# Optimization experiments

Hardware: AMD Instinct MI355X
Metric: run time of the kernel (lower is better)

The kernel has to match this reference:

```python
import jax, jax.numpy as jnp
import numpy as np

EPS_LN = 1e-12
EPS_BN = 1e-5


def layernorm(x, w, b):
    u = jnp.mean(x, axis=-1, keepdims=True)
    s = jnp.mean((x - u) ** 2, axis=-1, keepdims=True)
    return w * ((x - u) / jnp.sqrt(s + EPS_LN)) + b


def reps_block(x, ln1_w, ln1_b, lin_w, lin_b, ln2_w, ln2_b):
    # GRAPHLayerNorm -> (dropout, identity in eval) -> Linear -> ReLU -> GRAPHLayerNorm
    h = layernorm(x, ln1_w, ln1_b)
    h = jax.nn.relu(jnp.einsum('bnd,od->bno', h, lin_w) + lin_b)
    return layernorm(h, ln2_w, ln2_b)


def attend(x):
    # full dense self-attention: softmax(x x^T) x ; dropout is identity in eval
    scores = jnp.einsum('bnd,bmd->bnm', x, x)  # [B,4096,4096]
    attn = jax.nn.softmax(scores, axis=-1)
    return jnp.einsum('bnm,bmd->bnd', attn, x)


def setup_inputs() -> dict:
    key = jax.random.key(0)
    ks = jax.random.split(key, 8)
    B, C, H, W = 4, 512, 64, 64
    D = 512
    inp = {
        'T1': jax.random.normal(ks[0], (B, C, H, W), jnp.float32),
        'T2': jax.random.normal(ks[1], (B, C, H, W), jnp.float32),
        'w_conv3': jax.random.normal(ks[2], (1024, 1024, 3, 3), jnp.float32) * 0.01,
        'w_conv1': jax.random.normal(ks[3], (512, 1024, 1, 1), jnp.float32) * 0.03,
        'bn_gamma': jnp.ones((512,), jnp.float32),
        'bn_beta': jnp.zeros((512,), jnp.float32),
        'bn_mean': jnp.zeros((512,), jnp.float32),
        'bn_var': jnp.ones((512,), jnp.float32),
        'ln1_w': jnp.ones((D,), jnp.float32),
        'ln1_b': jnp.zeros((D,), jnp.float32),
        'lin_w': jax.random.normal(ks[4], (D, D), jnp.float32) * 0.04,
        'lin_b': jnp.zeros((D,), jnp.float32),
        'ln2_w': jnp.ones((D,), jnp.float32),
        'ln2_b': jnp.zeros((D,), jnp.float32),
    }
    return inp


def reference(T1, T2, w_conv3, w_conv1, bn_gamma, bn_beta, bn_mean, bn_var,
              ln1_w, ln1_b, lin_w, lin_b, ln2_w, ln2_b):
    B = T1.shape[0]
    X = jnp.concatenate((T1, T2), axis=1)  # [B,1024,64,64]
    dn = ('NCHW', 'OIHW', 'NCHW')
    X = jax.lax.conv_general_dilated(X, w_conv3, (1, 1), ((1, 1), (1, 1)), dimension_numbers=dn)
    X = jax.lax.conv_general_dilated(X, w_conv1, (1, 1), ((0, 0), (0, 0)), dimension_numbers=dn)  # [B,512,64,64]
    # BatchNorm (eval, running stats) + ReLU
    inv = (bn_gamma / jnp.sqrt(bn_var + EPS_BN))[None, :, None, None]
    X = jax.nn.relu(X * inv + (bn_beta - bn_mean * bn_gamma / jnp.sqrt(bn_var + EPS_BN))[None, :, None, None])
    x = X.transpose(0, 2, 3, 1).reshape(B, 4096, 512)
    # block 1
    rel = attend(x)
    rel = reps_block(x + rel, ln1_w, ln1_b, lin_w, lin_b, ln2_w, ln2_b)
    # block 2 (original code reuses self.reps_graph, i.e. SAME params)
    rel1 = attend(rel)
    rel1 = reps_block(rel + rel1, ln1_w, ln1_b, lin_w, lin_b, ln2_w, ln2_b)
    return rel1.reshape(B, 64, 64, 512).transpose(0, 3, 1, 2)  # [B,512,64,64]
```

## Files before the change

### kernel.cpp

```cpp
#include <hip/hip_runtime.h>
#include <stdint.h>

typedef float f32x4 __attribute__((ext_vector_type(4)));
typedef __bf16 bf16x8 __attribute__((ext_vector_type(8)));
typedef unsigned short u16;
typedef unsigned short u16x8 __attribute__((ext_vector_type(8)));

__device__ __forceinline__ float bf2f(u16 u){ unsigned int i = ((unsigned int)u)<<16; float f; __builtin_memcpy(&f,&i,4); return f; }
__device__ __forceinline__ u16 f2bf(float f){ unsigned int i; __builtin_memcpy(&i,&f,4); i += 0x7FFFu + ((i>>16)&1u); return (u16)(i>>16); }
__device__ __forceinline__ u16 f2h(float f){ _Float16 h = (_Float16)f; u16 b; __builtin_memcpy(&b,&h,2); return b; }
__device__ __forceinline__ float h2f(u16 b){ _Float16 h; __builtin_memcpy(&h,&b,2); return (float)h; }

__device__ __forceinline__ void gld16(const void* g, void* l){
  __builtin_amdgcn_global_load_lds(
      (const __attribute__((address_space(1))) void*)(uintptr_t)g,
      (__attribute__((address_space(3))) void*)(unsigned int)(uintptr_t)l, 16, 0, 0);
}

__global__ __launch_bounds__(256) void pad_interior(const float* __restrict__ T1,
                                                    const float* __restrict__ T2,
                                                    u16* __restrict__ Xpad){
  const int n = blockIdx.z, ct = blockIdx.y, pt = blockIdx.x;
  const int t = threadIdx.x;
  const int c0 = ct*64, p0 = pt*64;
  const float* src = (c0 < 512) ? (T1 + ((long)n*512 + c0)*4096)
                                : (T2 + ((long)n*512 + (c0-512))*4096);
  __shared__ u16 lds[64][66];
  #pragma unroll
  for (int i=0;i<4;i++){
    int c = i*16 + (t>>4);
    int ch = t&15;
    float4 v = *(const float4*)(src + (long)c*4096 + p0 + ch*4);
    int p = ch*4;
    lds[p+0][c] = f2bf(v.x); lds[p+1][c] = f2bf(v.y);
    lds[p+2][c] = f2bf(v.z); lds[p+3][c] = f2bf(v.w);
  }
  __syncthreads();
  #pragma unroll
  for (int i=0;i<8;i++){
    int p = i*8 + (t>>5);
    int c2 = t&31;
    int pix = p0 + p; int yy = (pix>>6)+1, xx = (pix&63)+1;
    ushort2 val; val.x = lds[p][2*c2]; val.y = lds[p][2*c2+1];
    *(ushort2*)(Xpad + (((long)n*66 + yy)*66 + xx)*1024 + c0 + 2*c2) = val;
  }
}

__global__ __launch_bounds__(256) void prep_w3(const float* __restrict__ w3, u16* __restrict__ wk3t){
  const int o = blockIdx.x; const int t = threadIdx.x;
  __shared__ u16 lds[9216];
  const float* src = w3 + (long)o*9216;
  #pragma unroll
  for (int i=0;i<9;i++){
    int j = i*256 + t;
    float4 v = *(const float4*)(src + j*4);
    lds[j*4+0]=f2bf(v.x); lds[j*4+1]=f2bf(v.y); lds[j*4+2]=f2bf(v.z); lds[j*4+3]=f2bf(v.w);
  }
  __syncthreads();
  u16* dst = wk3t + (long)o*9216;
  #pragma unroll
  for (int i=0;i<36;i++){
    int j = i*256 + t; int tp = j>>10, ci = j&1023;
    dst[j] = lds[ci*9+tp];
  }
}

__global__ void prep_w1(const float* __restrict__ w1, const float* __restrict__ bg,
                        const float* __restrict__ bv, u16* __restrict__ w1t){
  long i = (long)blockIdx.x*256 + threadIdx.x;
  int o = (int)(i>>10);
  float inv = bg[o] / sqrtf(bv[o] + 1e-5f);
  w1t[i] = f2bf(w1[i]*inv);
}

__global__ void prep_bias1(const float* __restrict__ bg, const float* __restrict__ bb,
                           const float* __restrict__ bm, const float* __restrict__ bv,
                           float* __restrict__ bias1){
  int o = blockIdx.x*256+threadIdx.x;
  float inv = bg[o]/sqrtf(bv[o]+1e-5f);
  bias1[o] = bb[o] - bm[o]*inv;
}

__global__ void cvt_bf(const float* __restrict__ s, u16* __restrict__ d){
  long i = (long)blockIdx.x*256 + threadIdx.x;
  d[i] = f2bf(s[i]);
}

__global__ __launch_bounds__(256) void row_norm(const u16* __restrict__ x, float* __restrict__ nrm){
  const int row = blockIdx.x*4 + (threadIdx.x>>6);
  const int lane = threadIdx.x & 63;
  u16x8 q = *(const u16x8*)(x + (long)row*512 + lane*8);
  float s = 0.f;
  #pragma unroll
  for (int j=0;j<8;j++){ float f = bf2f(q[j]); s += f*f; }
  #pragma unroll
  for (int off=32; off; off>>=1) s += __shfl_xor(s, off);
  if (lane==0) nrm[row] = s;
}

__global__ __launch_bounds__(256) void transpose_bf(const u16* __restrict__ src, u16* __restrict__ dst,
                                                    int R, int C, long sStr, long dStr){
  const int z = blockIdx.z;
  src += (long)z*sStr; dst += (long)z*dStr;
  const int r0 = blockIdx.x*64, c0 = blockIdx.y*64;
  const int t = threadIdx.x;
  __shared__ u16 lds[64][66];
  #pragma unroll
  for (int i=0;i<4;i++){
    int r = i*16 + (t>>4), ch = t&15;
    ushort4 v = *(const ushort4*)(src + (long)(r0+r)*C + c0 + ch*4);
    lds[r][ch*4+0]=v.x; lds[r][ch*4+1]=v.y; lds[r][ch*4+2]=v.z; lds[r][ch*4+3]=v.w;
  }
  __syncthreads();
  #pragma unroll
  for (int i=0;i<4;i++){
    int c = i*16 + (t>>4), ch = t&15;
    ushort4 v;
    v.x = lds[ch*4+0][c]; v.y = lds[ch*4+1][c]; v.z = lds[ch*4+2][c]; v.w = lds[ch*4+3][c];
    *(ushort4*)(dst + (long)(c0+c)*R + r0 + ch*4) = v;
  }
}

__global__ __launch_bounds__(256) void transpose_bf_f32(const u16* __restrict__ src, float* __restrict__ dst){
  const int z = blockIdx.z;
  src += (long)z*4096*512; dst += (long)z*512*4096;
  const int r0 = blockIdx.x*64, c0 = blockIdx.y*64;
  const int t = threadIdx.x;
  __shared__ u16 lds[64][66];
  #pragma unroll
  for (int i=0;i<4;i++){
    int r = i*16 + (t>>4), ch = t&15;
    ushort4 v = *(const ushort4*)(src + (long)(r0+r)*512 + c0 + ch*4);
    lds[r][ch*4+0]=v.x; lds[r][ch*4+1]=v.y; lds[r][ch*4+2]=v.z; lds[r][ch*4+3]=v.w;
  }
  __syncthreads();
  #pragma unroll
  for (int i=0;i<4;i++){
    int c = i*16 + (t>>4), ch = t&15;
    float4 v;
    v.x = bf2f(lds[ch*4+0][c]); v.y = bf2f(lds[ch*4+1][c]);
    v.z = bf2f(lds[ch*4+2][c]); v.w = bf2f(lds[ch*4+3][c]);
    *(float4*)(dst + (long)(c0+c)*4096 + r0 + ch*4) = v;
  }
}

template<int EPI, int CONV>
__global__ __launch_bounds__(512, 2) void gemm256(
    const u16* __restrict__ A, const u16* __restrict__ Bt, void* __restrict__ Cv,
    int K, int lda, int ldb, int ldc, const float* __restrict__ srow)
{
  extern __shared__ u16 sm[];
  const int t = threadIdx.x;
  const int lane = t & 63;
  const int wid = t >> 6;
  const int wr = wid >> 2, wc = wid & 3;

  const int orig = blockIdx.y * gridDim.x + blockIdx.x;
  const int cpx = (gridDim.x * gridDim.y) >> 3;
  const int swz = (orig & 7) * cpx + (orig >> 3);
  const int bx = swz % gridDim.x;
  const int by = swz / gridDim.x;
  const long m0 = (long)by * 256, n0 = (long)bx * 256;

  const int row0 = t >> 2;
  const int cs0  = (t & 3) ^ ((row0 >> 1) & 3);

  const u16 *aB0, *aB1;
  if (CONV) {
    long m_ = m0 + row0;
    long pb0 = ((long)((int)(m_>>12)*66 + (int)((m_>>6)&63)))*66 + (int)(m_&63);
    m_ = m0 + row0 + 128;
    long pb1 = ((long)((int)(m_>>12)*66 + (int)((m_>>6)&63)))*66 + (int)(m_&63);
    aB0 = A + pb0*1024 + cs0*8;
    aB1 = A + pb1*1024 + cs0*8;
  } else {
    aB0 = A + (m0 + row0)*(long)lda + cs0*8;
    aB1 = A + (m0 + row0 + 128)*(long)lda + cs0*8;
  }
  const u16* bB0 = Bt + (n0 + row0)*(long)ldb + cs0*8;
  const u16* bB1 = Bt + (n0 + row0 + 128)*(long)ldb + cs0*8;

  auto issueA = [&](int sub, long aoff){
    u16* d = sm + sub*8192 + t*8;
    gld16(aB0 + aoff, d);
    gld16(aB1 + aoff, d + 4096);
  };
  auto issueB = [&](int sub, long boff){
    u16* d = sm + 32768 + sub*8192 + t*8;
    gld16(bB0 + boff, d);
    gld16(bB1 + boff, d + 4096);
  };
  auto conv_aoff = [&](int tile)->long {
    int kb = tile << 6;
    int tap = kb >> 10;
    int cb  = kb & 1023;
    int ky = (tap >= 6) ? 2 : (tap >= 3 ? 1 : 0);
    int kx = tap - ky*3;
    return (long)(ky*66 + kx)*1024 + cb;
  };

  const int frow = lane & 15;
  const int elemoff = (((lane>>4) ^ ((frow>>1)&3)) << 3);
  const int rAoff = (wr*128 + frow)*32 + elemoff;
  const int rBoff = (wc*64  + frow)*32 + elemoff;

  f32x4 acc[8][4] = {};

  {
    long a0 = CONV ? conv_aoff(0) : 0L;
    issueA(0, a0);
    issueB(0, 0);
    issueA(1, a0 + 32);
    issueB(1, 32);
  }

  const int NT = K >> 6;
  for (int tile = 0; tile < NT; ++tile) {
    const int b = tile & 1;
    const int nb2 = b ^ 1;
    const bool lastT = (tile == NT-1);
    long aoffN = 0, boffN = 0;
    if (!lastT) {
      aoffN = CONV ? conv_aoff(tile+1) : (long)(tile+1)*64;
      boffN = (long)(tile+1)*64;
    }

    asm volatile("s_waitcnt vmcnt(4)" ::: "memory");
    __builtin_amdgcn_s_barrier();
    __builtin_amdgcn_sched_barrier(0);

    {
      const u16* pA = sm + (b*2+0)*8192 + rAoff;
      const u16* pB = sm + 32768 + (b*2+0)*8192 + rBoff;
      bf16x8 bf[4];
      #pragma unroll
      for (int i=0;i<4;i++) bf[i] = *(const bf16x8*)(pB + i*512);
      {
        bf16x8 a[4];
        #pragma unroll
        for (int i=0;i<4;i++) a[i] = *(const bf16x8*)(pA + i*512);
        if (!lastT) issueA(nb2*2+0, aoffN);
        __builtin_amdgcn_s_setprio(1);
        #pragma unroll
        for (int mi=0;mi<4;mi++)
          #pragma unroll
          for (int ni=0;ni<4;ni++)
            acc[mi][ni] = __builtin_amdgcn_mfma_f32_16x16x32_bf16(a[mi], bf[ni], acc[mi][ni],0,0,0);
        __builtin_amdgcn_s_setprio(0);
      }
      {
        bf16x8 a[4];
        #pragma unroll
        for (int i=0;i<4;i++) a[i] = *(const bf16x8*)(pA + (4+i)*512);
        if (!lastT) issueB(nb2*2+0, boffN);
        __builtin_amdgcn_s_setprio(1);
        #pragma unroll
        for (int mi=0;mi<4;mi++)
          #pragma unroll
          for (int ni=0;ni<4;ni++)
            acc[4+mi][ni] = __builtin_amdgcn_mfma_f32_16x16x32_bf16(a[mi], bf[ni], acc[4+mi][ni],0,0,0);
        __builtin_amdgcn_s_setprio(0);
      }
    }

    if (lastT) asm volatile("s_waitcnt vmcnt(0)" ::: "memory");
    else       asm volatile("s_waitcnt vmcnt(4)" ::: "memory");
    __builtin_amdgcn_s_barrier();
    __builtin_amdgcn_sched_barrier(0);

    {
      const u16* pA = sm + (b*2+1)*8192 + rAoff;
      const u16* pB = sm + 32768 + (b*2+1)*8192 + rBoff;
      bf16x8 bf[4];
      #pragma unroll
      for (int i=0;i<4;i++) bf[i] = *(const bf16x8*)(pB + i*512);
      {
        bf16x8 a[4];
        #pragma unroll
        for (int i=0;i<4;i++) a[i] = *(const bf16x8*)(pA + i*512);
        if (!lastT) issueA(nb2*2+1, aoffN + 32);
        __builtin_amdgcn_s_setprio(1);
        #pragma unroll
        for (int mi=0;mi<4;mi++)
          #pragma unroll
          for (int ni=0;ni<4;ni++)
            acc[mi][ni] = __builtin_amdgcn_mfma_f32_16x16x32_bf16(a[mi], bf[ni], acc[mi][ni],0,0,0);
        __builtin_amdgcn_s_setprio(0);
      }
      {
        bf16x8 a[4];
        #pragma unroll
        for (int i=0;i<4;i++) a[i] = *(const bf16x8*)(pA + (4+i)*512);
        if (!lastT) issueB(nb2*2+1, boffN + 32);
        __builtin_amdgcn_s_setprio(1);
        #pragma unroll
        for (int mi=0;mi<4;mi++)
          #pragma unroll
          for (int ni=0;ni<4;ni++)
            acc[4+mi][ni] = __builtin_amdgcn_mfma_f32_16x16x32_bf16(a[mi], bf[ni], acc[4+mi][ni],0,0,0);
        __builtin_amdgcn_s_setprio(0);
      }
    }
  }

  const int crow0 = wr*128 + ((lane>>4)<<2);
  const int ccol0 = wc*64 + frow;
  #pragma unroll
  for (int mi=0;mi<8;mi++){
    #pragma unroll
    for (int ni=0;ni<4;ni++){
      long col = n0 + ccol0 + ni*16;
      #pragma unroll
      for (int r=0;r<4;r++){
        long row = m0 + crow0 + mi*16 + r;
        float v = acc[mi][ni][r];
        if (EPI==3) ((u16*)Cv)[row*(long)ldc + col] = f2h(v - srow[row]);
        else        ((u16*)Cv)[row*(long)ldc + col] = f2bf(v);
      }
    }
  }
}

template<int EPI>
__global__ __launch_bounds__(256, 2) void gemm_bt(
    const u16* __restrict__ A, const u16* __restrict__ Bt,
    void* __restrict__ Cv, const float* __restrict__ bias,
    int K, int lda, int ldb, int ldc)
{
  const int t = threadIdx.x;
  const int lane = t & 63;
  const int w = t >> 6;
  const int wr = w >> 1, wc = w & 1;
  const long m0 = (long)blockIdx.y * 128;
  const long n0 = (long)blockIdx.x * 128;

  __shared__ u16 lA[128*32];
  __shared__ u16 lB[128*32];

  const u16* aS0 = A + (m0 + (t>>2))*(long)lda + (t&3)*8;
  const u16* aS1 = aS0 + 64*(long)lda;
  const u16* bS0 = Bt + (n0 + (t>>2))*(long)ldb + (t&3)*8;
  const u16* bS1 = bS0 + 64*(long)ldb;
  u16* dA0 = lA + t*8; u16* dA1 = lA + 2048 + t*8;
  u16* dB0 = lB + t*8; u16* dB1 = lB + 2048 + t*8;

  f32x4 acc[4][4] = {};
  const int frow = lane & 15, kq = (lane >> 4) * 8;
  const u16* rA = lA + (wr*64 + frow)*32 + kq;
  const u16* rB = lB + (wc*64 + frow)*32 + kq;

  for (int kb = 0; kb < K; kb += 32) {
    gld16(aS0 + kb, dA0); gld16(aS1 + kb, dA1);
    gld16(bS0 + kb, dB0); gld16(bS1 + kb, dB1);
    __syncthreads();
    bf16x8 af[4], bfr[4];
    #pragma unroll
    for (int i=0;i<4;i++) af[i]  = *(const bf16x8*)(rA + i*512);
    #pragma unroll
    for (int i=0;i<4;i++) bfr[i] = *(const bf16x8*)(rB + i*512);
    #pragma unroll
    for (int mi=0;mi<4;mi++)
      #pragma unroll
      for (int ni=0;ni<4;ni++)
        acc[mi][ni] = __builtin_amdgcn_mfma_f32_16x16x32_bf16(af[mi], bfr[ni], acc[mi][ni], 0,0,0);
    __syncthreads();
  }

  const int crow0 = wr*64 + ((lane>>4)<<2);
  const int ccol0 = wc*64 + (lane&15);
  #pragma unroll
  for (int mi=0;mi<4;mi++){
    #pragma unroll
    for (int ni=0;ni<4;ni++){
      long col = n0 + ccol0 + ni*16;
      float bv = (EPI==1) ? bias[col] : 0.0f;
      #pragma unroll
      for (int r=0;r<4;r++){
        long row = m0 + crow0 + mi*16 + r;
        float v = acc[mi][ni][r];
        if (EPI==1){ v += bv; v = v > 0.0f ? v : 0.0f; }
        ((u16*)Cv)[row*(long)ldc + col] = f2bf(v);
      }
    }
  }
}

__global__ __launch_bounds__(256, 2) void pv_gemm(
    const u16* __restrict__ P0, const u16* __restrict__ P1,
    const u16* __restrict__ P2, const u16* __restrict__ P3,
    const u16* __restrict__ xT, u16* __restrict__ attb)
{
  const int L = blockIdx.x;
  const int xcd = L & 7;
  const int z = xcd >> 1;
  const int tile = ((L >> 3) << 1) + (xcd & 1);
  const int bx = tile & 3, by = tile >> 2;
  const long ZS = 4096L*512;
  const u16* A  = (z==0)?P0:(z==1)?P1:(z==2)?P2:P3;
  const u16* Bt = xT   + (long)z*ZS;
  u16*       C  = attb + (long)z*ZS;
  const int K = 4096, lda = 4096, ldb = 4096, ldc = 512;

  const int t = threadIdx.x;
  const int lane = t & 63;
  const int w = t >> 6;
  const int wr = w >> 1, wc = w & 1;
  const long m0 = (long)by * 128;
  const long n0 = (long)bx * 128;

  __shared__ u16 lA[128*32];
  __shared__ u16 lB[128*32];

  const u16* aS0 = A + (m0 + (t>>2))*(long)lda + (t&3)*8;
  const u16* aS1 = aS0 + 64*(long)lda;
  const u16* bS0 = Bt + (n0 + (t>>2))*(long)ldb + (t&3)*8;
  const u16* bS1 = bS0 + 64*(long)ldb;
  u16* dA0 = lA + t*8; u16* dA1 = lA + 2048 + t*8;
  u16* dB0 = lB + t*8; u16* dB1 = lB + 2048 + t*8;

  f32x4 acc[4][4] = {};
  const int frow = lane & 15, kq = (lane >> 4) * 8;
  const u16* rA = lA + (wr*64 + frow)*32 + kq;
  const u16* rB = lB + (wc*64 + frow)*32 + kq;

  for (int kb = 0; kb < K; kb += 32) {
    gld16(aS0 + kb, dA0); gld16(aS1 + kb, dA1);
    gld16(bS0 + kb, dB0); gld16(bS1 + kb, dB1);
    __syncthreads();
    bf16x8 af[4], bfr[4];
    #pragma unroll
    for (int i=0;i<4;i++) af[i]  = *(const bf16x8*)(rA + i*512);
    #pragma unroll
    for (int i=0;i<4;i++) bfr[i] = *(const bf16x8*)(rB + i*512);
    #pragma unroll
    for (int mi=0;mi<4;mi++)
      #pragma unroll
      for (int ni=0;ni<4;ni++)
        acc[mi][ni] = __builtin_amdgcn_mfma_f32_16x16x32_bf16(af[mi], bfr[ni], acc[mi][ni], 0,0,0);
    __syncthreads();
  }

  const int crow0 = wr*64 + ((lane>>4)<<2);
  const int ccol0 = wc*64 + (lane&15);
  #pragma unroll
  for (int mi=0;mi<4;mi++){
    #pragma unroll
    for (int ni=0;ni<4;ni++){
      long col = n0 + ccol0 + ni*16;
      #pragma unroll
      for (int r=0;r<4;r++){
        long row = m0 + crow0 + mi*16 + r;
        C[row*(long)ldc + col] = f2bf(acc[mi][ni][r]);
      }
    }
  }
}

__global__ __launch_bounds__(256) void softmax_row(const u16* __restrict__ S, u16* __restrict__ P){
  const long row = blockIdx.x;
  const u16* src = S + row*4096;
  const int t = threadIdx.x, lane = t&63, w = t>>6;
  float v[16];
  #pragma unroll
  for (int i=0;i<2;i++){
    u16x8 q = *(const u16x8*)(src + t*16 + i*8);
    #pragma unroll
    for (int j=0;j<8;j++) v[i*8+j] = h2f(q[j]);
  }
  float mx = v[0];
  #pragma unroll
  for (int i=1;i<16;i++) mx = fmaxf(mx, v[i]);
  #pragma unroll
  for (int off=32; off; off>>=1) mx = fmaxf(mx, __shfl_xor(mx, off));
  __shared__ float red[4];
  if (lane==0) red[w] = mx;
  __syncthreads();
  mx = fmaxf(fmaxf(red[0],red[1]), fmaxf(red[2],red[3]));
  float sum = 0.0f;
  #pragma unroll
  for (int i=0;i<16;i++){ v[i] = __expf(v[i]-mx); sum += v[i]; }
  #pragma unroll
  for (int off=32; off; off>>=1) sum += __shfl_xor(sum, off);
  __shared__ float red2[4];
  if (lane==0) red2[w] = sum;
  __syncthreads();
  sum = red2[0]+red2[1]+red2[2]+red2[3];
  const float inv = 1.0f/sum;
  u16* dst = P + row*4096;
  #pragma unroll
  for (int i=0;i<2;i++){
    u16x8 o;
    #pragma unroll
    for (int j=0;j<8;j++) o[j] = f2bf(v[i*8+j]*inv);
    *(u16x8*)(dst + t*16 + i*8) = o;
  }
}

template<int ADD>
__global__ __launch_bounds__(256) void ln_row(
    const u16* __restrict__ X, const u16* __restrict__ Y,
    const float* __restrict__ w, const float* __restrict__ b,
    u16* __restrict__ outB)
{
  const long row = blockIdx.x;
  const int t = threadIdx.x, lane = t&63, wv = t>>6;
  ushort2 xv = *(const ushort2*)(X + row*512 + t*2);
  float v0 = bf2f(xv.x), v1 = bf2f(xv.y);
  if (ADD){
    ushort2 yv = *(const ushort2*)(Y + row*512 + t*2);
    v0 += bf2f(yv.x); v1 += bf2f(yv.y);
  }
  float s = v0+v1, q = v0*v0 + v1*v1;
  #pragma unroll
  for (int off=32; off; off>>=1){ s += __shfl_xor(s,off); q += __shfl_xor(q,off); }
  __shared__ float red[8];
  if (lane==0){ red[wv]=s; red[4+wv]=q; }
  __syncthreads();
  s = red[0]+red[1]+red[2]+red[3];
  q = red[4]+red[5]+red[6]+red[7];
  const float u = s*(1.0f/512.0f);
  const float var = q*(1.0f/512.0f) - u*u;
  const float inv = rsqrtf(var + 1e-12f);
  const int c = t*2;
  float o0 = (v0-u)*inv*w[c]   + b[c];
  float o1 = (v1-u)*inv*w[c+1] + b[c+1];
  ushort2 ov; ov.x=f2bf(o0); ov.y=f2bf(o1);
  *(ushort2*)(outB + row*512 + c) = ov;
}

extern "C" void kernel_launch(void* const* d_in, const int* in_sizes, int n_in,
                              void* d_out, int out_size, void* d_ws, size_t ws_size,
                              hipStream_t stream) {
  const float* T1   = (const float*)d_in[0];
  const float* T2   = (const float*)d_in[1];
  const float* w3   = (const float*)d_in[2];
  const float* w1   = (const float*)d_in[3];
  const float* bg   = (const float*)d_in[4];
  const float* bb   = (const float*)d_in[5];
  const float* bm   = (const float*)d_in[6];
  const float* bv   = (const float*)d_in[7];
  const float* ln1w = (const float*)d_in[8];
  const float* ln1b = (const float*)d_in[9];
  const float* linw = (const float*)d_in[10];
  const float* linb = (const float*)d_in[11];
  const float* ln2w = (const float*)d_in[12];
  const float* ln2b = (const float*)d_in[13];

  hipFuncSetAttribute(reinterpret_cast<const void*>(gemm256<0,1>),
                      hipFuncAttributeMaxDynamicSharedMemorySize, 131072);
  hipFuncSetAttribute(reinterpret_cast<const void*>(gemm256<3,0>),
                      hipFuncAttributeMaxDynamicSharedMemorySize, 131072);

  char* ws = (char*)d_ws;
  size_t off = 0;
  auto alloc = [&](size_t bytes)->char* {
    char* p = ws + off;
    off += (bytes + 255) & ~(size_t)255;
    return p;
  };
  const size_t XPAD_B = 4L*66*66*1024*2;
  u16*   Xpad  = (u16*)  alloc(XPAD_B);
  u16*   wk3t  = (u16*)  alloc(1024L*9216*2);
  u16*   w1t   = (u16*)  alloc(512L*1024*2);
  u16*   lint  = (u16*)  alloc(512L*512*2);
  float* bias1 = (float*)alloc(512*4);
  float* nrm   = (float*)alloc(16384L*4);
  u16*   Y1    = (u16*)  alloc(16384L*1024*2);
  u16*   x0    = (u16*)  alloc(16384L*512*2);
  u16*   xT    = (u16*)  alloc(4L*512*4096*2);
  u16*   Sreg  = (u16*)  alloc(2L*4096*4096*2);
  u16*   attb  = (u16*)  alloc(16384L*512*2);
  u16*   h     = (u16*)  alloc(16384L*512*2);
  u16*   g     = (u16*)  alloc(16384L*512*2);
  u16*   rel1  = (u16*)  alloc(16384L*512*2);
  u16*   Sh    = Sreg;
  u16*   P0    = Y1;
  u16*   P1    = h;
  u16*   P2    = Sreg + 4096L*4096;
  u16*   P3    = Xpad;
  if (off > ws_size) return;

  const long ZS = 4096L*512;

  hipMemsetAsync(Xpad, 0, XPAD_B, stream);
  pad_interior<<<dim3(64,16,4), 256, 0, stream>>>(T1, T2, Xpad);
  prep_w3<<<1024, 256, 0, stream>>>(w3, wk3t);
  prep_w1<<<2048, 256, 0, stream>>>(w1, bg, bv, w1t);
  prep_bias1<<<2, 256, 0, stream>>>(bg, bb, bm, bv, bias1);
  cvt_bf<<<1024, 256, 0, stream>>>(linw, lint);

  gemm256<0,1><<<dim3(4,64), 512, 131072, stream>>>(Xpad, wk3t, (void*)Y1, 9216, 0, 9216, 1024,
                                                    nullptr);
  gemm_bt<1><<<dim3(4,128), 256, 0, stream>>>(Y1, w1t, (void*)x0, bias1, 1024, 1024, 1024, 512);

  u16* Pz[4] = {P0, P1, P2, P3};
  auto attend = [&](const u16* xin){
    transpose_bf<<<dim3(64,8,4), 256, 0, stream>>>(xin, xT, 4096, 512, ZS, ZS);
    row_norm<<<4096, 256, 0, stream>>>(xin, nrm);
    for (int z=0; z<4; z++){
      const u16* xz = xin + (long)z*ZS;
      gemm256<3,0><<<dim3(16,16), 512, 131072, stream>>>(xz, xz, (void*)Sh, 512, 512, 512, 4096,
                                                         nrm + (long)z*4096);
      softmax_row<<<4096, 256, 0, stream>>>(Sh, Pz[z]);
    }
    pv_gemm<<<512, 256, 0, stream>>>(P0, P1, P2, P3, xT, attb);
  };

  attend(x0);
  ln_row<1><<<16384, 256, 0, stream>>>(x0, attb, ln1w, ln1b, h);
  gemm_bt<1><<<dim3(4,128), 256, 0, stream>>>(h, lint, (void*)g, linb, 512, 512, 512, 512);
  ln_row<0><<<16384, 256, 0, stream>>>(g, nullptr, ln2w, ln2b, rel1);

  attend(rel1);
  ln_row<1><<<16384, 256, 0, stream>>>(rel1, attb, ln1w, ln1b, h);
  gemm_bt<1><<<dim3(4,128), 256, 0, stream>>>(h, lint, (void*)g, linb, 512, 512, 512, 512);
  ln_row<0><<<16384, 256, 0, stream>>>(g, nullptr, ln2w, ln2b, x0);

  transpose_bf_f32<<<dim3(64,8,4), 256, 0, stream>>>(x0, (float*)d_out);
}
```

Measured before the change: 911.2 us.

## Pipeline PV GEMM with multi-buffered async LDS loads and swizzled layout

Rewrites the P·V GEMM main loop to prefetch the next K-tiles into a four-slot LDS ring (64 KB dynamic shared memory) using async global-to-LDS loads. It synchronises with vmcnt waits and raw barriers instead of two __syncthreads per step. An XOR swizzle on the LDS column chunks is meant to reduce bank conflicts, and s_setprio brackets the MFMA blocks. The goal is to hide global load latency behind MFMA work. The cost is more LDS per block, which may limit occupancy, plus hand-managed wait counts that must stay correct.

```diff
diff --git a/kernel.cpp b/kernel.cpp
--- a/kernel.cpp
+++ b/kernel.cpp
@@ -385,11 +385,12 @@
   }
 }
 
-__global__ __launch_bounds__(256, 2) void pv_gemm(
+__global__ __launch_bounds__(256, 2) void pv5(
     const u16* __restrict__ P0, const u16* __restrict__ P1,
     const u16* __restrict__ P2, const u16* __restrict__ P3,
     const u16* __restrict__ xT, u16* __restrict__ attb)
 {
+  extern __shared__ u16 pm[];
   const int L = blockIdx.x;
   const int xcd = L & 7;
   const int z = xcd >> 1;
@@ -399,49 +400,129 @@
   const u16* A  = (z==0)?P0:(z==1)?P1:(z==2)?P2:P3;
   const u16* Bt = xT   + (long)z*ZS;
   u16*       C  = attb + (long)z*ZS;
-  const int K = 4096, lda = 4096, ldb = 4096, ldc = 512;
+  const long m0 = (long)by * 128, n0 = (long)bx * 128;
 
   const int t = threadIdx.x;
   const int lane = t & 63;
   const int w = t >> 6;
   const int wr = w >> 1, wc = w & 1;
-  const long m0 = (long)by * 128;
-  const long n0 = (long)bx * 128;
-
-  __shared__ u16 lA[128*32];
-  __shared__ u16 lB[128*32];
-
-  const u16* aS0 = A + (m0 + (t>>2))*(long)lda + (t&3)*8;
-  const u16* aS1 = aS0 + 64*(long)lda;
-  const u16* bS0 = Bt + (n0 + (t>>2))*(long)ldb + (t&3)*8;
-  const u16* bS1 = bS0 + 64*(long)ldb;
-  u16* dA0 = lA + t*8; u16* dA1 = lA + 2048 + t*8;
-  u16* dB0 = lB + t*8; u16* dB1 = lB + 2048 + t*8;
+
+  const int row0 = t >> 2;
+  const int cs0  = (t & 3) ^ ((row0 >> 1) & 3);
+
+  const u16* aB0 = A + (m0 + row0)*4096L + cs0*8;
+  const u16* aB1 = aB0 + 64*4096L;
+  const u16* bB0 = Bt + (n0 + row0)*4096L + cs0*8;
+  const u16* bB1 = bB0 + 64*4096L;
+
+  auto issueA = [&](int sub, long off){
+    u16* d = pm + sub*4096 + t*8;
+    gld16(aB0 + off, d);
+    gld16(aB1 + off, d + 2048);
+  };
+  auto issueB = [&](int sub, long off){
+    u16* d = pm + 16384 + sub*4096 + t*8;
+    gld16(bB0 + off, d);
+    gld16(bB1 + off, d + 2048);
+  };
+
+  const int frow = lane & 15;
+  const int elemoff = (((lane>>4) ^ ((frow>>1)&3)) << 3);
+  const int rAoff = (wr*64 + frow)*32 + elemoff;
+  const int rBoff = (wc*64 + frow)*32 + elemoff;
 
   f32x4 acc[4][4] = {};
-  const int frow = lane & 15, kq = (lane >> 4) * 8;
-  const u16* rA = lA + (wr*64 + frow)*32 + kq;
-  const u16* rB = lB + (wc*64 + frow)*32 + kq;
-
-  for (int kb = 0; kb < K; kb += 32) {
-    gld16(aS0 + kb, dA0); gld16(aS1 + kb, dA1);
-    gld16(bS0 + kb, dB0); gld16(bS1 + kb, dB1);
-    __syncthreads();
-    bf16x8 af[4], bfr[4];
-    #pragma unroll
-    for (int i=0;i<4;i++) af[i]  = *(const bf16x8*)(rA + i*512);
-    #pragma unroll
-    for (int i=0;i<4;i++) bfr[i] = *(const bf16x8*)(rB + i*512);
-    #pragma unroll
-    for (int mi=0;mi<4;mi++)
+
+  issueA(0, 0);  issueB(0, 0);
+  issueA(1, 32); issueB(1, 32);
+
+  const int NT = 64;
+  for (int tl = 0; tl < NT; ++tl) {
+    const int b = tl & 1;
+    const int nb2 = b ^ 1;
+    const bool lastT = (tl == NT-1);
+    const long offN = (long)(tl+1)*64;
+
+    asm volatile("s_waitcnt vmcnt(4)" ::: "memory");
+    __builtin_amdgcn_s_barrier();
+    __builtin_amdgcn_sched_barrier(0);
+
+    {
+      const u16* pA = pm + (b*2+0)*4096 + rAoff;
+      const u16* pB = pm + 16384 + (b*2+0)*4096 + rBoff;
+      bf16x8 bf[4];
       #pragma unroll
-      for (int ni=0;ni<4;ni++)
-        acc[mi][ni] = __builtin_amdgcn_mfma_f32_16x16x32_bf16(af[mi], bfr[ni], acc[mi][ni], 0,0,0);
-    __syncthreads();
+      for (int i=0;i<4;i++) bf[i] = *(const bf16x8*)(pB + i*512);
+      {
+        bf16x8 a[2];
+        #pragma unroll
+        for (int i=0;i<2;i++) a[i] = *(const bf16x8*)(pA + i*512);
+        if (!lastT) issueA(nb2*2+0, offN);
+        __builtin_amdgcn_s_setprio(1);
+        #pragma unroll
+        for (int mi=0;mi<2;mi++)
+          #pragma unroll
+          for (int ni=0;ni<4;ni++)
+            acc[mi][ni] = __builtin_amdgcn_mfma_f32_16x16x32_bf16(a[mi], bf[ni], acc[mi][ni],0,0,0);
+        __builtin_amdgcn_s_setprio(0);
+      }
+      {
+        bf16x8 a[2];
+        #pragma unroll
+        for (int i=0;i<2;i++) a[i] = *(const bf16x8*)(pA + (2+i)*512);
+        if (!lastT) issueB(nb2*2+0, offN);
+        __builtin_amdgcn_s_setprio(1);
+        #pragma unroll
+        for (int mi=0;mi<2;mi++)
+          #pragma unroll
+          for (int ni=0;ni<4;ni++)
+            acc[2+mi][ni] = __builtin_amdgcn_mfma_f32_16x16x32_bf16(a[mi], bf[ni], acc[2+mi][ni],0,0,0);
+        __builtin_amdgcn_s_setprio(0);
+      }
+    }
+
+    if (lastT) asm volatile("s_waitcnt vmcnt(0)" ::: "memory");
+    else       asm volatile("s_waitcnt vmcnt(4)" ::: "memory");
+    __builtin_amdgcn_s_barrier();
+    __builtin_amdgcn_sched_barrier(0);
+
+    {
+      const u16* pA = pm + (b*2+1)*4096 + rAoff;
+      const u16* pB = pm + 16384 + (b*2+1)*4096 + rBoff;
+      bf16x8 bf[4];
+      #pragma unroll
+      for (int i=0;i<4;i++) bf[i] = *(const bf16x8*)(pB + i*512);
+      {
+        bf16x8 a[2];
+        #pragma unroll
+        for (int i=0;i<2;i++) a[i] = *(const bf16x8*)(pA + i*512);
+        if (!lastT) issueA(nb2*2+1, offN + 32);
+        __builtin_amdgcn_s_setprio(1);
+        #pragma unroll
+        for (int mi=0;mi<2;mi++)
+          #pragma unroll
+          for (int ni=0;ni<4;ni++)
+            acc[mi][ni] = __builtin_amdgcn_mfma_f32_16x16x32_bf16(a[mi], bf[ni], acc[mi][ni],0,0,0);
+        __builtin_amdgcn_s_setprio(0);
+      }
+      {
+        bf16x8 a[2];
+        #pragma unroll
+        for (int i=0;i<2;i++) a[i] = *(const bf16x8*)(pA + (2+i)*512);
+        if (!lastT) issueB(nb2*2+1, offN + 32);
+        __builtin_amdgcn_s_setprio(1);
+        #pragma unroll
+        for (int mi=0;mi<2;mi++)
+          #pragma unroll
+          for (int ni=0;ni<4;ni++)
+            acc[2+mi][ni] = __builtin_amdgcn_mfma_f32_16x16x32_bf16(a[mi], bf[ni], acc[2+mi][ni],0,0,0);
+        __builtin_amdgcn_s_setprio(0);
+      }
+    }
   }
 
   const int crow0 = wr*64 + ((lane>>4)<<2);
-  const int ccol0 = wc*64 + (lane&15);
+  const int ccol0 = wc*64 + frow;
   #pragma unroll
   for (int mi=0;mi<4;mi++){
     #pragma unroll
@@ -450,7 +531,7 @@
       #pragma unroll
       for (int r=0;r<4;r++){
         long row = m0 + crow0 + mi*16 + r;
-        C[row*(long)ldc + col] = f2bf(acc[mi][ni][r]);
+        C[row*512 + col] = f2bf(acc[mi][ni][r]);
       }
     }
   }
@@ -550,6 +631,8 @@
                       hipFuncAttributeMaxDynamicSharedMemorySize, 131072);
   hipFuncSetAttribute(reinterpret_cast<const void*>(gemm256<3,0>),
                       hipFuncAttributeMaxDynamicSharedMemorySize, 131072);
+  hipFuncSetAttribute(reinterpret_cast<const void*>(pv5),
+                      hipFuncAttributeMaxDynamicSharedMemorySize, 65536);
 
   char* ws = (char*)d_ws;
   size_t off = 0;
@@ -603,7 +686,7 @@
                                                          nrm + (long)z*4096);
       softmax_row<<<4096, 256, 0, stream>>>(Sh, Pz[z]);
     }
-    pv_gemm<<<512, 256, 0, stream>>>(P0, P1, P2, P3, xT, attb);
+    pv5<<<512, 256, 65536, stream>>>(P0, P1, P2, P3, xT, attb);
   };
 
   attend(x0);
```

Measured after the change: 893.1 us. 2.0% less time.
